# Performance work log

Hardware: AMD Instinct MI355X
Metric: run time of the kernel (lower is better)

Reference implementation:

```python
import jax, jax.numpy as jnp
import numpy as np

N, E, F, H, L, G, C = 50000, 800000, 64, 128, 4, 64, 10
GAMMA = 10.0  # Gaussian RBF width for centers in (0,1)
CENTERS = jnp.linspace(0.0, 1.0, H)


def _ssp(v):
    # shifted softplus, SchNet's nonlinearity
    return jax.nn.softplus(v) - 0.6931472


def setup_inputs() -> dict:
    key = jax.random.key(0)
    ks = jax.random.split(key, 20)

    def w(k, shape, fan_in):
        return (jax.random.normal(k, shape, dtype=jnp.float32) / np.sqrt(fan_in)).astype(jnp.float32)

    x = jax.random.normal(ks[0], (N, F), dtype=jnp.float32)
    edge_dist = jax.random.uniform(ks[1], (E,), dtype=jnp.float32)
    edge_src = jax.random.randint(ks[2], (E,), 0, N, dtype=jnp.int32)
    edge_dst = jax.random.randint(ks[3], (E,), 0, N, dtype=jnp.int32)
    graph_ids = jnp.sort(jax.random.randint(ks[4], (N,), 0, G, dtype=jnp.int32))

    return {
        "x": x, "edge_dist": edge_dist,
        "edge_src": edge_src, "edge_dst": edge_dst, "graph_ids": graph_ids,
        # first-layer node projection F->H, remaining layers H->H (stacked)
        "W1_0": w(ks[5], (F, H), F), "b1_0": jnp.zeros((H,), jnp.float32),
        "W1_rest": w(ks[6], (L - 1, H, H), H), "b1_rest": jnp.zeros((L - 1, H), jnp.float32),
        # filter-generating MLP on RBF features, per layer
        "Wf1": w(ks[7], (L, H, H), H), "bf1": jnp.zeros((L, H), jnp.float32),
        "Wf2": w(ks[8], (L, H, H), H), "bf2": jnp.zeros((L, H), jnp.float32),
        # output projection per layer
        "W2": w(ks[9], (L, H, H), H), "b2": jnp.zeros((L, H), jnp.float32),
        # readout FC
        "fc_w": w(ks[10], (H, C), H), "fc_b": jnp.zeros((C,), jnp.float32),
    }


def _schnet_conv(x, rbf, src, dst, W1, b1, Wf1, bf1, Wf2, bf2, W2, b2):
    # CFConv: project nodes, gate gathered source features with a distance
    # filter, scatter-sum to destinations, project out.
    filt = _ssp(rbf @ Wf1 + bf1) @ Wf2 + bf2          # [E, H]
    h = x @ W1 + b1                                    # [N, H]
    msg = h[src] * filt                                # [E, H] gather + gate
    agg = jax.ops.segment_sum(msg, dst, num_segments=N)  # [N, H] scatter-sum
    return agg @ W2 + b2


def reference(x, edge_dist, edge_src, edge_dst, graph_ids,
              W1_0, b1_0, W1_rest, b1_rest, Wf1, bf1, Wf2, bf2, W2, b2,
              fc_w, fc_b):
    # Gaussian radial basis expansion of edge distances, shared across layers
    rbf = jnp.exp(-GAMMA * (edge_dist[:, None] - CENTERS) ** 2)  # [E, H]

    h = jax.nn.relu(_schnet_conv(x, rbf, edge_src, edge_dst,
                                 W1_0, b1_0, Wf1[0], bf1[0], Wf2[0], bf2[0],
                                 W2[0], b2[0]))
    for i in range(L - 1):
        h = jax.nn.relu(_schnet_conv(h, rbf, edge_src, edge_dst,
                                     W1_rest[i], b1_rest[i],
                                     Wf1[i + 1], bf1[i + 1],
                                     Wf2[i + 1], bf2[i + 1],
                                     W2[i + 1], b2[i + 1]))

    # dgl.mean_nodes: per-graph mean over nodes
    sums = jax.ops.segment_sum(h, graph_ids, num_segments=G)           # [G, H]
    cnts = jax.ops.segment_sum(jnp.ones((N,), h.dtype), graph_ids, num_segments=G)
    pooled = sums / jnp.maximum(cnts, 1.0)[:, None]

    logits = pooled @ fc_w + fc_b                                       # [G, C]
    return jax.nn.log_softmax(logits, axis=1)
```

## Files before the change

kernel.cpp:

```cpp
#include <hip/hip_runtime.h>
#include <math.h>

#define NN 50000
#define EE 800000
#define FF 64
#define HH 128
#define LL 4
#define GG 64
#define CC 10
#define TT 512
#define TTP 513
#define BD 64
#define ABLK 1024
#define EPB 782
#define SEGC 192
#define SUBB 96
#define SRW 6250

#define PB_CVTW 8
#define PB_TAB ((TT / 16) * LL)
#define PB_CVTX (NN * FF / 4 / 256)
#define PB_PART ABLK

#define SCB (8 * SUBB)
#define GEMMB (NN / 16)

typedef unsigned short ushort_t;
typedef unsigned int uint_t;

typedef short s8v __attribute__((ext_vector_type(8)));
typedef float f32x4 __attribute__((ext_vector_type(4)));

__device__ inline ushort_t f2bf(float f) {
  uint_t u = __float_as_uint(f);
  uint_t r = (u + 0x7FFFu + ((u >> 16) & 1u)) >> 16;
  return (ushort_t)r;
}
__device__ inline float bf1f(ushort_t v) { return __uint_as_float(((uint_t)v) << 16); }

__device__ inline ushort_t f2h(float f) {
  union { _Float16 h[2]; ushort_t us[2]; } c;
  c.h[0] = (_Float16)f;
  return c.us[0];
}
__device__ inline float h_lo(uint_t u) {
  union { uint_t w; _Float16 h[2]; } c; c.w = u; return (float)c.h[0];
}
__device__ inline float h_hi(uint_t u) {
  union { uint_t w; _Float16 h[2]; } c; c.w = u; return (float)c.h[1];
}

__global__ __launch_bounds__(256) void prep(
    const float* __restrict__ x, ushort_t* __restrict__ xb,
    const float* __restrict__ W1_0, const float* __restrict__ W1_rest,
    const float* __restrict__ W2, ushort_t* __restrict__ wt,
    const float* __restrict__ Wf1, const float* __restrict__ bf1,
    const float* __restrict__ Wf2, const float* __restrict__ bf2,
    ushort_t* __restrict__ tables,
    const int* __restrict__ dst, const int* __restrict__ src,
    const float* __restrict__ dist,
    uint2* __restrict__ seg, int* __restrict__ segcnt, int* __restrict__ bcnt,
    const int* __restrict__ gid, int* __restrict__ gcnt, float* __restrict__ gsum) {
  __shared__ float rbf[16][HH];
  __shared__ float hid[16][HH];
  __shared__ int lcnt[8];
  int tid = threadIdx.x;
  int b = blockIdx.x;

  if (b < PB_CVTW) {
    int mid = b;
    const float* srcm; int K;
    if (mid == 0) { srcm = W1_0; K = FF; }
    else if (mid < 4) { srcm = W1_rest + (size_t)(mid - 1) * HH * HH; K = HH; }
    else { srcm = W2 + (size_t)(mid - 4) * HH * HH; K = HH; }
    ushort_t* dstm = wt + (size_t)mid * HH * HH;
    for (int idx = tid; idx < K * HH; idx += 256) {
      int k = idx >> 7, n = idx & 127;
      dstm[n * K + k] = f2bf(srcm[idx]);
    }
  } else if (b < PB_CVTW + PB_TAB) {
    int bb = b - PB_CVTW;
    int l = bb & 3;
    int tb = (bb >> 2) * 16;
    int j = tid & 127;
    float c = j * (1.0f / (HH - 1));
#pragma unroll
    for (int tt2 = 0; tt2 < 16; ++tt2) {
      float d = (tb + tt2) * (1.0f / (TT - 1));
      float dd = d - c;
      rbf[tt2][j] = expf(-10.0f * dd * dd);
    }
    __syncthreads();
    const float* W1f = Wf1 + (size_t)l * HH * HH;
    float s[16];
    float bb1 = bf1[l * HH + j];
#pragma unroll
    for (int tt2 = 0; tt2 < 16; ++tt2) s[tt2] = bb1;
    for (int k = 0; k < HH; ++k) {
      float wk = W1f[(size_t)k * HH + j];
#pragma unroll
      for (int tt2 = 0; tt2 < 16; ++tt2) s[tt2] += rbf[tt2][k] * wk;
    }
#pragma unroll
    for (int tt2 = 0; tt2 < 16; ++tt2)
      hid[tt2][j] = fmaxf(s[tt2], 0.f) + log1pf(expf(-fabsf(s[tt2]))) - 0.6931472f;
    __syncthreads();
    const float* W2f = Wf2 + (size_t)l * HH * HH;
    float bb2 = bf2[l * HH + j];
#pragma unroll
    for (int tt2 = 0; tt2 < 16; ++tt2) s[tt2] = bb2;
    for (int k = 0; k < HH; ++k) {
      float wk = W2f[(size_t)k * HH + j];
#pragma unroll
      for (int tt2 = 0; tt2 < 16; ++tt2) s[tt2] += hid[tt2][k] * wk;
    }
    if (tid < 128) {
#pragma unroll
      for (int tt2 = 0; tt2 < 16; ++tt2)
        tables[((size_t)l * TTP + 1 + tb + tt2) * HH + j] = f2h(s[tt2]);
    }
  } else if (b < PB_CVTW + PB_TAB + PB_CVTX) {
    int i = (b - PB_CVTW - PB_TAB) * 256 + tid;
    const float4* x4 = (const float4*)x;
    float4 v = x4[i];
    union { ushort_t us[4]; uint2 u; } pk;
    pk.us[0] = f2bf(v.x); pk.us[1] = f2bf(v.y); pk.us[2] = f2bf(v.z); pk.us[3] = f2bf(v.w);
    *(uint2*)&xb[i * 4] = pk.u;
  } else if (b < PB_CVTW + PB_TAB + PB_CVTX + PB_PART) {
    int pb = b - PB_CVTW - PB_TAB - PB_CVTX;
    if (tid < 8) lcnt[tid] = 0;
    int z = pb * 49 + tid;
    if (tid < 49 && z < NN) bcnt[z] = 0;
    __syncthreads();
    int e0 = pb * EPB;
    int e1 = min(e0 + EPB, EE);
    for (int e = e0 + tid; e < e1; e += 256) {
      int d = __builtin_nontemporal_load(dst + e);
      int s = __builtin_nontemporal_load(src + e);
      float di = __builtin_nontemporal_load(dist + e);
      float u = di * (float)(TT - 1);
      int t0 = (int)(fminf(fmaxf(u, 0.f), (float)(TT - 1)) + 0.5f);
      if (t0 > TT - 1) t0 = TT - 1;
      int r = d / SRW;
      int pos = atomicAdd(&lcnt[r], 1);
      if (pos < SEGC)
        seg[((size_t)(r << 10) + pb) * SEGC + pos] =
            make_uint2((uint_t)d, ((uint_t)s << 10) | (uint_t)(t0 + 1));
    }
    __syncthreads();
    if (tid < 8) segcnt[(tid << 10) + pb] = min(lcnt[tid], SEGC);
  } else {
    for (int i = tid; i < GG * HH; i += 256) gsum[i] = 0.f;
    for (int i = tid; i < LL * HH; i += 256)
      tables[(size_t)(i >> 7) * TTP * HH + (i & 127)] = 0;
    if (tid < GG) {
      int g = tid;
      int lo = 0, hi = NN;
      while (lo < hi) { int m = (lo + hi) >> 1; if (gid[m] < g) lo = m + 1; else hi = m; }
      int b0 = lo;
      lo = 0; hi = NN;
      int g1 = g + 1;
      while (lo < hi) { int m = (lo + hi) >> 1; if (gid[m] < g1) lo = m + 1; else hi = m; }
      gcnt[g] = lo - b0;
    }
  }
}

__global__ __launch_bounds__(256) void scatter_gemm1(
    const uint2* __restrict__ seg, const int* __restrict__ segcnt,
    int* __restrict__ bcnt, uint_t* __restrict__ epad,
    const ushort_t* __restrict__ xb, const ushort_t* __restrict__ wt,
    const float* __restrict__ b1_0, ushort_t* __restrict__ pbuf) {
  int tid = threadIdx.x;
  if (blockIdx.x < SCB) {
    int r = blockIdx.x & 7;
    int sub = blockIdx.x >> 3;
    for (int b = sub; b < ABLK; b += SUBB) {
      int cnt = segcnt[(r << 10) + b];
      const uint_t* sp = (const uint_t*)(seg + ((size_t)(r << 10) + b) * SEGC);
      for (int i = tid; i < cnt; i += 256) {
        uint_t ex = __builtin_nontemporal_load(sp + i * 2);
        uint_t ey = __builtin_nontemporal_load(sp + i * 2 + 1);
        int slot = atomicAdd(&bcnt[ex], 1);
        if (slot < BD) epad[(size_t)ex * BD + slot] = ey;
      }
    }
  } else {
    int tile = blockIdx.x - SCB;
    int lane = tid & 63, wave = tid >> 6, m = lane & 15, quad = lane >> 4;
    int rowbase = tile * 16, colbase = wave * 32;
    const ushort_t* arow = xb + (size_t)(rowbase + m) * FF;
    const ushort_t* brow0 = wt + (size_t)(colbase + m) * FF;
    const ushort_t* brow1 = wt + (size_t)(colbase + 16 + m) * FF;
    f32x4 acc0 = {0.f, 0.f, 0.f, 0.f};
    f32x4 acc1 = {0.f, 0.f, 0.f, 0.f};
    for (int kc = 0; kc < FF; kc += 32) {
      int k = kc + quad * 8;
      union { uint4 u; s8v v; } a, b0, b1;
      a.u  = *(const uint4*)(arow + k);
      b0.u = *(const uint4*)(brow0 + k);
      b1.u = *(const uint4*)(brow1 + k);
      acc0 = __builtin_amdgcn_mfma_f32_16x16x32_bf16(a.v, b0.v, acc0, 0, 0, 0);
      acc1 = __builtin_amdgcn_mfma_f32_16x16x32_bf16(a.v, b1.v, acc1, 0, 0, 0);
    }
    float bb0 = b1_0[colbase + m];
    float bb1 = b1_0[colbase + 16 + m];
#pragma unroll
    for (int reg = 0; reg < 4; ++reg) {
      int row = rowbase + quad * 4 + reg;
      pbuf[(size_t)row * HH + colbase + m] = f2h(acc0[reg] + bb0);
      pbuf[(size_t)row * HH + colbase + 16 + m] = f2h(acc1[reg] + bb1);
    }
  }
}

__global__ __launch_bounds__(512) void fused_layer(
    const ushort_t* __restrict__ pIn, const ushort_t* __restrict__ table,
    const uint_t* __restrict__ epad, const int* __restrict__ bcnt,
    const ushort_t* __restrict__ WT2, const float* __restrict__ b2l,
    const ushort_t* __restrict__ WT1, const float* __restrict__ b1l,
    ushort_t* __restrict__ OUT, int last) {
  __shared__ ushort_t At[16 * 128];
  __shared__ ushort_t T[16 * 128];
  int tid = threadIdx.x;
  int lane = tid & 63;
  int wv = tid >> 6;
  int tile = blockIdx.x;
  const uint_t* pu = (const uint_t*)pIn;
  const uint_t* tu = (const uint_t*)table;

  int baseV = tile * 16 + wv * 2;
  uint_t ed[2];
  float ax[2], ay[2];
  int B = 0;
#pragma unroll
  for (int i = 0; i < 2; ++i) {
    int n = min(bcnt[baseV + i], BD);
    ed[i] = (lane < n) ? epad[(size_t)(baseV + i) * BD + lane] : 0u;
    B = max(B, (n + 3) >> 2);
    ax[i] = 0.f; ay[i] = 0.f;
  }
  for (int c = 0; c < B; ++c) {
    uint_t pv[2][4], fv[2][4];
#pragma unroll
    for (int i = 0; i < 2; ++i) {
#pragma unroll
      for (int k = 0; k < 4; ++k) {
        uint_t e = (uint_t)__builtin_amdgcn_readlane((int)ed[i], c * 4 + k);
        pv[i][k] = pu[(size_t)(e >> 10) * 64 + lane];
        fv[i][k] = tu[(size_t)(e & 1023u) * 64 + lane];
      }
    }
#pragma unroll
    for (int i = 0; i < 2; ++i) {
#pragma unroll
      for (int k = 0; k < 4; ++k) {
        ax[i] += h_lo(pv[i][k]) * h_lo(fv[i][k]);
        ay[i] += h_hi(pv[i][k]) * h_hi(fv[i][k]);
      }
    }
  }
#pragma unroll
  for (int i = 0; i < 2; ++i) {
    int r = wv * 2 + i;
    uint_t packed = (uint_t)f2bf(ax[i]) | ((uint_t)f2bf(ay[i]) << 16);
    ((uint_t*)At)[r * 64 + (((lane >> 2) ^ r) << 2) + (lane & 3)] = packed;
  }
  __syncthreads();
  int m = lane & 15, quad = lane >> 4;
  int rowbase = tile * 16, colbase = wv * 16;
  {
    const ushort_t* brow0 = WT2 + (size_t)(colbase + m) * HH;
    f32x4 acc0 = {0.f, 0.f, 0.f, 0.f};
    for (int kc = 0; kc < HH; kc += 32) {
      int k = kc + quad * 8;
      int g = k >> 3;
      union { uint4 u; s8v v; } a, b0;
      a.u = *(const uint4*)&At[m * 128 + ((g ^ m) << 3)];
      b0.u = *(const uint4*)(brow0 + k);
      acc0 = __builtin_amdgcn_mfma_f32_16x16x32_bf16(a.v, b0.v, acc0, 0, 0, 0);
    }
    float bb0 = b2l[colbase + m];
    if (last) {
#pragma unroll
      for (int reg = 0; reg < 4; ++reg) {
        int row = rowbase + quad * 4 + reg;
        OUT[(size_t)row * HH + colbase + m] = f2bf(fmaxf(acc0[reg] + bb0, 0.f));
      }
      return;
    }
#pragma unroll
    for (int reg = 0; reg < 4; ++reg) {
      int r = quad * 4 + reg;
      float v0 = fmaxf(acc0[reg] + bb0, 0.f);
      int c0 = colbase + m;
      T[r * 128 + (((c0 >> 3) ^ r) << 3) + (c0 & 7)] = f2bf(v0);
    }
  }
  __syncthreads();
  {
    const ushort_t* brow0 = WT1 + (size_t)(colbase + m) * HH;
    f32x4 acc0 = {0.f, 0.f, 0.f, 0.f};
    for (int kc = 0; kc < HH; kc += 32) {
      int k0 = kc + quad * 8;
      int g = k0 >> 3;
      union { uint4 u; s8v v; } a, b0;
      a.u = *(const uint4*)&T[m * 128 + ((g ^ m) << 3)];
      b0.u = *(const uint4*)(brow0 + k0);
      acc0 = __builtin_amdgcn_mfma_f32_16x16x32_bf16(a.v, b0.v, acc0, 0, 0, 0);
    }
    float bb0 = b1l[colbase + m];
#pragma unroll
    for (int reg = 0; reg < 4; ++reg) {
      int row = rowbase + quad * 4 + reg;
      OUT[(size_t)row * HH + colbase + m] = f2h(acc0[reg] + bb0);
    }
  }
}

__global__ __launch_bounds__(128) void pool_kernel(const ushort_t* __restrict__ h, const int* __restrict__ gid,
                                                   float* __restrict__ gsum) {
  int j = threadIdx.x;
  int i0 = blockIdx.x * 128;
  int i1 = min(i0 + 128, NN);
  if (i0 >= NN) return;
  float acc = 0.f;
  int gcur = gid[i0];
  for (int i = i0; i < i1; ++i) {
    int g = gid[i];
    if (g != gcur) {
      atomicAdd(&gsum[gcur * HH + j], acc);
      acc = 0.f;
      gcur = g;
    }
    acc += bf1f(h[(size_t)i * HH + j]);
  }
  atomicAdd(&gsum[gcur * HH + j], acc);
}

__global__ __launch_bounds__(128) void final_kernel(const float* __restrict__ gsum, const int* __restrict__ gcnt,
                                                    const float* __restrict__ fc_w, const float* __restrict__ fc_b,
                                                    float* __restrict__ out) {
  int g = blockIdx.x, j = threadIdx.x;
  __shared__ float pooled[HH];
  __shared__ float logits[CC];
  __shared__ float lse;
  float cnt = fmaxf((float)gcnt[g], 1.0f);
  pooled[j] = gsum[g * HH + j] / cnt;
  __syncthreads();
  if (j < CC) {
    float s = fc_b[j];
    for (int k = 0; k < HH; ++k) s += pooled[k] * fc_w[k * CC + j];
    logits[j] = s;
  }
  __syncthreads();
  if (j == 0) {
    float m = -1e30f;
    for (int c = 0; c < CC; ++c) m = fmaxf(m, logits[c]);
    float s = 0.f;
    for (int c = 0; c < CC; ++c) s += expf(logits[c] - m);
    lse = m + logf(s);
  }
  __syncthreads();
  if (j < CC) out[g * CC + j] = logits[j] - lse;
}

extern "C" void kernel_launch(void* const* d_in, const int* in_sizes, int n_in,
                              void* d_out, int out_size, void* d_ws, size_t ws_size,
                              hipStream_t stream) {
  const float* x       = (const float*)d_in[0];
  const float* edist   = (const float*)d_in[1];
  const int*   esrc    = (const int*)d_in[2];
  const int*   edst    = (const int*)d_in[3];
  const int*   gid     = (const int*)d_in[4];
  const float* W1_0    = (const float*)d_in[5];
  const float* b1_0    = (const float*)d_in[6];
  const float* W1_rest = (const float*)d_in[7];
  const float* b1_rest = (const float*)d_in[8];
  const float* Wf1     = (const float*)d_in[9];
  const float* bf1     = (const float*)d_in[10];
  const float* Wf2     = (const float*)d_in[11];
  const float* bf2     = (const float*)d_in[12];
  const float* W2      = (const float*)d_in[13];
  const float* b2      = (const float*)d_in[14];
  const float* fc_w    = (const float*)d_in[15];
  const float* fc_b    = (const float*)d_in[16];
  float* out = (float*)d_out;

  char* ws = (char*)d_ws;
  size_t o = 0;
  auto alloc = [&](size_t bytes) {
    void* p = ws + o;
    o += (bytes + 255) & ~(size_t)255;
    return p;
  };
  ushort_t* tables = (ushort_t*)alloc(sizeof(ushort_t) * (size_t)LL * TTP * HH);
  ushort_t* xb     = (ushort_t*)alloc(sizeof(ushort_t) * (size_t)NN * FF);
  ushort_t* wt     = (ushort_t*)alloc(sizeof(ushort_t) * 8 * HH * HH);
  ushort_t* pbuf   = (ushort_t*)alloc(sizeof(ushort_t) * (size_t)NN * HH);
  ushort_t* pbuf2  = (ushort_t*)alloc(sizeof(ushort_t) * (size_t)NN * HH);
  ushort_t* hbuf   = (ushort_t*)alloc(sizeof(ushort_t) * (size_t)NN * HH);
  int*      bcnt   = (int*)alloc(sizeof(int) * NN);
  uint_t*   epad   = (uint_t*)alloc(sizeof(uint_t) * (size_t)NN * BD);
  uint2*    seg    = (uint2*)alloc(sizeof(uint2) * (size_t)8 * ABLK * SEGC);
  int*      segcnt = (int*)alloc(sizeof(int) * 8 * ABLK);
  float*    gsum   = (float*)alloc(sizeof(float) * GG * HH);
  int*      gcnt   = (int*)alloc(sizeof(int) * GG);

  const int prepBlocks = PB_CVTW + PB_TAB + PB_CVTX + PB_PART + 1;
  prep<<<prepBlocks, 256, 0, stream>>>(x, xb, W1_0, W1_rest, W2, wt,
                                       Wf1, bf1, Wf2, bf2, tables,
                                       edst, esrc, edist, seg, segcnt, bcnt,
                                       gid, gcnt, gsum);
  scatter_gemm1<<<SCB + GEMMB, 256, 0, stream>>>(seg, segcnt, bcnt, epad,
                                                 xb, wt, b1_0, pbuf);

  ushort_t* pIn = pbuf;
  ushort_t* pOut = pbuf2;
  for (int l = 0; l < LL; ++l) {
    int last = (l == LL - 1);
    fused_layer<<<GEMMB, 512, 0, stream>>>(
        pIn, tables + (size_t)l * TTP * HH, epad, bcnt,
        wt + (size_t)(4 + l) * HH * HH, b2 + (size_t)l * HH,
        last ? nullptr : (wt + (size_t)(1 + l) * HH * HH),
        last ? nullptr : (b1_rest + (size_t)l * HH),
        last ? hbuf : pOut, last);
    ushort_t* tmp = pIn; pIn = pOut; pOut = tmp;
  }

  pool_kernel<<<(NN + 127) / 128, 128, 0, stream>>>(hbuf, gid, gsum);
  final_kernel<<<GG, 128, 0, stream>>>(gsum, gcnt, fc_w, fc_b, out);
}
```

Baseline: 397.8 us.

## Stage halved filter table in LDS and gather two edges per wave with 64-bit loads

Cuts the distance-filter lookup table from 512 to 256 bins so one layer's fp16 table (about 64KB) fits in shared memory. Each fused_layer block now copies the table into LDS with an XOR swizzle, and the per-edge filter reads come from LDS instead of global memory. The gather loop is restructured so each half-wave handles a different edge using 64-bit loads, and the two halves are combined with a cross-lane shuffle. The trade-offs are coarser filter quantisation, which costs accuracy, plus a 64KB table copy per block that limits occupancy and adds load traffic for every tile.

```diff
diff --git a/kernel.cpp b/kernel.cpp
--- a/kernel.cpp
+++ b/kernel.cpp
@@ -8,8 +8,8 @@
 #define LL 4
 #define GG 64
 #define CC 10
-#define TT 512
-#define TTP 513
+#define TT 256
+#define TTP 257
 #define BD 64
 #define ABLK 1024
 #define EPB 782
@@ -27,6 +27,7 @@
 
 typedef unsigned short ushort_t;
 typedef unsigned int uint_t;
+typedef unsigned long long u64_t;
 
 typedef short s8v __attribute__((ext_vector_type(8)));
 typedef float f32x4 __attribute__((ext_vector_type(4)));
@@ -59,7 +60,7 @@
     ushort_t* __restrict__ tables,
     const int* __restrict__ dst, const int* __restrict__ src,
     const float* __restrict__ dist,
-    uint2* __restrict__ seg, int* __restrict__ segcnt, int* __restrict__ bcnt,
+    uint_t* __restrict__ seg, int* __restrict__ segcnt, int* __restrict__ bcnt,
     const int* __restrict__ gid, int* __restrict__ gcnt, float* __restrict__ gsum) {
   __shared__ float rbf[16][HH];
   __shared__ float hid[16][HH];
@@ -123,9 +124,9 @@
     int i = (b - PB_CVTW - PB_TAB) * 256 + tid;
     const float4* x4 = (const float4*)x;
     float4 v = x4[i];
-    union { ushort_t us[4]; uint2 u; } pk;
+    union { ushort_t us[4]; u64_t u; } pk;
     pk.us[0] = f2bf(v.x); pk.us[1] = f2bf(v.y); pk.us[2] = f2bf(v.z); pk.us[3] = f2bf(v.w);
-    *(uint2*)&xb[i * 4] = pk.u;
+    *(u64_t*)&xb[i * 4] = pk.u;
   } else if (b < PB_CVTW + PB_TAB + PB_CVTX + PB_PART) {
     int pb = b - PB_CVTW - PB_TAB - PB_CVTX;
     if (tid < 8) lcnt[tid] = 0;
@@ -143,9 +144,11 @@
       if (t0 > TT - 1) t0 = TT - 1;
       int r = d / SRW;
       int pos = atomicAdd(&lcnt[r], 1);
-      if (pos < SEGC)
-        seg[((size_t)(r << 10) + pb) * SEGC + pos] =
-            make_uint2((uint_t)d, ((uint_t)s << 10) | (uint_t)(t0 + 1));
+      if (pos < SEGC) {
+        uint_t* sp = seg + (((size_t)(r << 10) + pb) * SEGC + pos) * 2;
+        sp[0] = (uint_t)d;
+        sp[1] = ((uint_t)s << 9) | (uint_t)(t0 + 1);
+      }
     }
     __syncthreads();
     if (tid < 8) segcnt[(tid << 10) + pb] = min(lcnt[tid], SEGC);
@@ -167,7 +170,7 @@
 }
 
 __global__ __launch_bounds__(256) void scatter_gemm1(
-    const uint2* __restrict__ seg, const int* __restrict__ segcnt,
+    const uint_t* __restrict__ seg, const int* __restrict__ segcnt,
     int* __restrict__ bcnt, uint_t* __restrict__ epad,
     const ushort_t* __restrict__ xb, const ushort_t* __restrict__ wt,
     const float* __restrict__ b1_0, ushort_t* __restrict__ pbuf) {
@@ -177,7 +180,7 @@
     int sub = blockIdx.x >> 3;
     for (int b = sub; b < ABLK; b += SUBB) {
       int cnt = segcnt[(r << 10) + b];
-      const uint_t* sp = (const uint_t*)(seg + ((size_t)(r << 10) + b) * SEGC);
+      const uint_t* sp = seg + ((size_t)(r << 10) + b) * SEGC * 2;
       for (int i = tid; i < cnt; i += 256) {
         uint_t ex = __builtin_nontemporal_load(sp + i * 2);
         uint_t ey = __builtin_nontemporal_load(sp + i * 2 + 1);
@@ -215,56 +218,78 @@
 }
 
 __global__ __launch_bounds__(512) void fused_layer(
-    const ushort_t* __restrict__ pIn, const ushort_t* __restrict__ table,
+    const ushort_t* __restrict__ pIn, const ushort_t* __restrict__ tabG,
     const uint_t* __restrict__ epad, const int* __restrict__ bcnt,
     const ushort_t* __restrict__ WT2, const float* __restrict__ b2l,
     const ushort_t* __restrict__ WT1, const float* __restrict__ b1l,
     ushort_t* __restrict__ OUT, int last) {
+  __shared__ ushort_t Tab[TTP * HH];
   __shared__ ushort_t At[16 * 128];
   __shared__ ushort_t T[16 * 128];
   int tid = threadIdx.x;
   int lane = tid & 63;
   int wv = tid >> 6;
   int tile = blockIdx.x;
-  const uint_t* pu = (const uint_t*)pIn;
-  const uint_t* tu = (const uint_t*)table;
+  int l32 = lane & 31;
+
+  {
+    const u64_t* g = (const u64_t*)tabG;
+    u64_t* s = (u64_t*)Tab;
+    for (int i = tid; i < (TTP * HH) / 4; i += 512) {
+      int row = i >> 5, j = i & 31;
+      s[(row << 5) + (j ^ (row & 31))] = g[i];
+    }
+  }
 
   int baseV = tile * 16 + wv * 2;
   uint_t ed[2];
-  float ax[2], ay[2];
+  float a0[2], a1[2], a2[2], a3[2];
   int B = 0;
 #pragma unroll
   for (int i = 0; i < 2; ++i) {
     int n = min(bcnt[baseV + i], BD);
     ed[i] = (lane < n) ? epad[(size_t)(baseV + i) * BD + lane] : 0u;
-    B = max(B, (n + 3) >> 2);
-    ax[i] = 0.f; ay[i] = 0.f;
-  }
+    B = max(B, (n + 1) >> 1);
+    a0[i] = 0.f; a1[i] = 0.f; a2[i] = 0.f; a3[i] = 0.f;
+  }
+  __syncthreads();
+
+  const u64_t* pu = (const u64_t*)pIn;
+  const u64_t* tu = (const u64_t*)Tab;
+  bool hi = lane >= 32;
   for (int c = 0; c < B; ++c) {
-    uint_t pv[2][4], fv[2][4];
 #pragma unroll
     for (int i = 0; i < 2; ++i) {
-#pragma unroll
-      for (int k = 0; k < 4; ++k) {
-        uint_t e = (uint_t)__builtin_amdgcn_readlane((int)ed[i], c * 4 + k);
-        pv[i][k] = pu[(size_t)(e >> 10) * 64 + lane];
-        fv[i][k] = tu[(size_t)(e & 1023u) * 64 + lane];
-      }
-    }
+      uint_t eA = (uint_t)__builtin_amdgcn_readlane((int)ed[i], 2 * c);
+      uint_t eB = (uint_t)__builtin_amdgcn_readlane((int)ed[i], 2 * c + 1);
+      uint_t e = hi ? eB : eA;
+      union { u64_t u; uint_t w[2]; } pv, fv;
+      pv.u = pu[(size_t)(e >> 9) * 32 + l32];
+      uint_t trow = e & 511u;
+      fv.u = tu[(trow << 5) + (l32 ^ (trow & 31u))];
+      a0[i] += h_lo(pv.w[0]) * h_lo(fv.w[0]);
+      a1[i] += h_hi(pv.w[0]) * h_hi(fv.w[0]);
+      a2[i] += h_lo(pv.w[1]) * h_lo(fv.w[1]);
+      a3[i] += h_hi(pv.w[1]) * h_hi(fv.w[1]);
+    }
+  }
+#pragma unroll
+  for (int i = 0; i < 2; ++i) {
+    a0[i] += __shfl_xor(a0[i], 32);
+    a1[i] += __shfl_xor(a1[i], 32);
+    a2[i] += __shfl_xor(a2[i], 32);
+    a3[i] += __shfl_xor(a3[i], 32);
+  }
+  if (lane < 32) {
 #pragma unroll
     for (int i = 0; i < 2; ++i) {
-#pragma unroll
-      for (int k = 0; k < 4; ++k) {
-        ax[i] += h_lo(pv[i][k]) * h_lo(fv[i][k]);
-        ay[i] += h_hi(pv[i][k]) * h_hi(fv[i][k]);
-      }
-    }
-  }
-#pragma unroll
-  for (int i = 0; i < 2; ++i) {
-    int r = wv * 2 + i;
-    uint_t packed = (uint_t)f2bf(ax[i]) | ((uint_t)f2bf(ay[i]) << 16);
-    ((uint_t*)At)[r * 64 + (((lane >> 2) ^ r) << 2) + (lane & 3)] = packed;
+      int r = wv * 2 + i;
+      int d0 = l32 * 2, d1 = d0 + 1;
+      ((uint_t*)At)[r * 64 + (((d0 >> 2) ^ r) << 2) + (d0 & 3)] =
+          (uint_t)f2bf(a0[i]) | ((uint_t)f2bf(a1[i]) << 16);
+      ((uint_t*)At)[r * 64 + (((d1 >> 2) ^ r) << 2) + (d1 & 3)] =
+          (uint_t)f2bf(a2[i]) | ((uint_t)f2bf(a3[i]) << 16);
+    }
   }
   __syncthreads();
   int m = lane & 15, quad = lane >> 4;
@@ -402,7 +427,7 @@
   ushort_t* hbuf   = (ushort_t*)alloc(sizeof(ushort_t) * (size_t)NN * HH);
   int*      bcnt   = (int*)alloc(sizeof(int) * NN);
   uint_t*   epad   = (uint_t*)alloc(sizeof(uint_t) * (size_t)NN * BD);
-  uint2*    seg    = (uint2*)alloc(sizeof(uint2) * (size_t)8 * ABLK * SEGC);
+  uint_t*   seg    = (uint_t*)alloc(sizeof(uint_t) * (size_t)2 * 8 * ABLK * SEGC);
   int*      segcnt = (int*)alloc(sizeof(int) * 8 * ABLK);
   float*    gsum   = (float*)alloc(sizeof(float) * GG * HH);
   int*      gcnt   = (int*)alloc(sizeof(int) * GG);
```

Result: slower. 552.7 us (+38.9%).
